# Performance work log

Measured on AMD Instinct MI355X. Metric: run time of the kernel, lower is better.

## Reference

```python
import jax, jax.numpy as jnp
import numpy as np

CHUNK = 128


def setup_inputs() -> dict:
    key = jax.random.key(0)
    ks = jax.random.split(key, 10)
    B, L, d, n = 4, 2048, 192, 64
    sd = 1.0 / np.sqrt(d)
    return {
        "x": jax.random.normal(ks[0], (B, L, d), dtype=jnp.float32),
        "A_log": -jnp.log(2.0) + 0.1 * jax.random.normal(ks[1], (d,), dtype=jnp.float32),
        "W_B": sd * jax.random.normal(ks[2], (n, d), dtype=jnp.float32),
        "W_C": sd * jax.random.normal(ks[3], (n, d), dtype=jnp.float32),
        "W_dt": sd * jax.random.normal(ks[4], (d, d), dtype=jnp.float32),
        "b_dt": 0.1 * jax.random.normal(ks[5], (d,), dtype=jnp.float32),
        "W_xp": sd * jax.random.normal(ks[6], (2 * d, d), dtype=jnp.float32),
        "b_xp": 0.1 * jax.random.normal(ks[7], (2 * d,), dtype=jnp.float32),
        "W_out": sd * jax.random.normal(ks[8], (d, d), dtype=jnp.float32),
        "b_out": 0.1 * jax.random.normal(ks[9], (d,), dtype=jnp.float32),
    }


def reference(x, A_log, W_B, W_C, W_dt, b_dt, W_xp, b_xp, W_out, b_out):
    p = CHUNK
    b, l, d = x.shape
    n = W_B.shape[0]
    pad = (-l) % p
    xp = jnp.pad(x, ((0, 0), (0, pad), (0, 0))) if pad > 0 else x
    c = xp.shape[1] // p

    A = -jnp.exp(A_log)                                   # (d,)
    proj = xp @ W_xp.T + b_xp                             # (b, Lp, 2d)
    x_bar, z = jnp.split(proj, 2, axis=-1)
    Bm = x_bar @ W_B.T                                    # (b, Lp, n)
    Cm = x_bar @ W_C.T                                    # (b, Lp, n)
    dt = jax.nn.softplus(x_bar @ W_dt.T + b_dt)           # (b, Lp, d)
    A_bar = jnp.exp(dt * A)                               # (b, Lp, d)

    resh = lambda t: t.reshape(b, c, p, t.shape[-1])
    xc, Bc, Cc, Ac = resh(x_bar), resh(Bm), resh(Cm), resh(A_bar)

    # intra-chunk: masked decay matrix M[b,c,i,j,d]
    log_A = jnp.log(jnp.abs(Ac) + 1e-8)
    la_cum = jnp.cumsum(log_A, axis=2)                    # (b,c,p,d)
    log_M = la_cum[:, :, :, None, :] - la_cum[:, :, None, :, :]
    causal = jnp.tril(jnp.ones((p, p), dtype=x.dtype))
    M = jnp.exp(log_M) * causal[None, None, :, :, None]   # (b,c,p,p,d)
    G = jnp.einsum('bcin,bcjn->bcij', Cc, Bc)             # C_i . B_j
    # same math as einsum('bcpn,bcpnd->bcpd', C, einsum('bcijd,bcjnd->bcind', M, B x))
    y_intra = jnp.einsum('bcij,bcijd,bcjd->bcid', G, M, xc)

    # inter-chunk recurrence over chunk states
    chunk_A = jnp.prod(Ac, axis=2)                        # (b,c,d)
    chunk_states = jnp.einsum('bcpn,bcpd->bcnd', Bc, xc * Ac)

    def step(state, inp):
        ca, cs = inp                                       # (b,d), (b,n,d)
        return state * ca[:, None, :] + cs, state          # emit state BEFORE update

    _, prev = jax.lax.scan(
        step,
        jnp.zeros((b, n, d), dtype=x.dtype),
        (jnp.moveaxis(chunk_A, 1, 0), jnp.moveaxis(chunk_states, 1, 0)),
    )
    prev = jnp.moveaxis(prev, 0, 1)                       # (b,c,n,d)
    y_inter = jnp.einsum('bcpn,bcnd->bcpd', Cc, prev)

    y = (y_intra + y_inter).reshape(b, c * p, d)[:, :l]
    y = y * jax.nn.silu(z[:, :l])
    return y @ W_out.T + b_out
```

## Files before the change

kernel.cpp:

```cpp
#include <hip/hip_runtime.h>
#include <math.h>

#define TOK      8192
#define DIM      192
#define NST      64
#define PCHUNK   128
#define NCHUNKS  64
#define CPB      16
#define BATCH    4
#define NG       4
#define NPG      16
#define SUB      32
#define NSUB     4

typedef __attribute__((ext_vector_type(8))) short  bf16x8;
typedef __attribute__((ext_vector_type(4))) float  f32x4;

__device__ __forceinline__ unsigned short f2bf(float f) {
    unsigned int u = __float_as_uint(f);
    u += 0x7fff + ((u >> 16) & 1);
    return (unsigned short)(u >> 16);
}
__device__ __forceinline__ float bf2f(unsigned short h) {
    return __uint_as_float(((unsigned int)h) << 16);
}

__global__ __launch_bounds__(256)
void cast_kernel(const float* __restrict__ x,   const float* __restrict__ Wxp,
                 const float* __restrict__ WB,  const float* __restrict__ WC,
                 const float* __restrict__ Wdt, const float* __restrict__ Wout,
                 unsigned short* __restrict__ xb,     unsigned short* __restrict__ wxpb,
                 unsigned short* __restrict__ wbcdtb, unsigned short* __restrict__ woutb)
{
    int u = blockIdx.x * 256 + threadIdx.x;
    const float* src; unsigned short* dst; int idx;
    if      (u < 393216) { src = x;    dst = xb;             idx = u; }
    else if (u < 411648) { src = Wxp;  dst = wxpb;           idx = u - 393216; }
    else if (u < 414720) { src = WB;   dst = wbcdtb;         idx = u - 411648; }
    else if (u < 417792) { src = WC;   dst = wbcdtb + 12288; idx = u - 414720; }
    else if (u < 427008) { src = Wdt;  dst = wbcdtb + 24576; idx = u - 417792; }
    else if (u < 436224) { src = Wout; dst = woutb;          idx = u - 427008; }
    else return;
    float4 v = *(const float4*)(src + (size_t)idx * 4);
    ushort4 r; r.x = f2bf(v.x); r.y = f2bf(v.y); r.z = f2bf(v.z); r.w = f2bf(v.w);
    *(ushort4*)(dst + (size_t)idx * 4) = r;
}

__device__ __forceinline__
void mfma_64x64(const unsigned short* __restrict__ X, int ldx,
                const unsigned short* __restrict__ W, int K,
                int m_wave, int n0, int lr, int kg, f32x4 acc[4][4])
{
    for (int k0 = 0; k0 < K; k0 += 32) {
        bf16x8 af[4], bfr[4];
        #pragma unroll
        for (int mi = 0; mi < 4; ++mi)
            af[mi] = *(const bf16x8*)(X + (size_t)(m_wave + mi*16 + lr) * ldx + k0 + kg*8);
        #pragma unroll
        for (int ni = 0; ni < 4; ++ni)
            bfr[ni] = *(const bf16x8*)(W + (size_t)(n0 + ni*16 + lr) * K + k0 + kg*8);
        #pragma unroll
        for (int mi = 0; mi < 4; ++mi)
            #pragma unroll
            for (int ni = 0; ni < 4; ++ni)
                acc[mi][ni] = __builtin_amdgcn_mfma_f32_16x16x32_bf16(
                                  af[mi], bfr[ni], acc[mi][ni], 0, 0, 0);
    }
}

__global__ __launch_bounds__(256)
void proj_gemm(const unsigned short* __restrict__ xb,
               const unsigned short* __restrict__ wxpb,
               const float* __restrict__ b_xp,
               float* __restrict__ proj, unsigned short* __restrict__ projb)
{
    const int lane = threadIdx.x & 63, wave = threadIdx.x >> 6;
    const int m_wave = blockIdx.x * 256 + wave * 64;
    const int n0 = blockIdx.y * 64;
    const int lr = lane & 15, kg = lane >> 4;
    f32x4 acc[4][4] = {};
    mfma_64x64(xb, DIM, wxpb, DIM, m_wave, n0, lr, kg, acc);
    #pragma unroll
    for (int ni = 0; ni < 4; ++ni) {
        int col = n0 + ni*16 + lr;
        float bias = b_xp[col];
        #pragma unroll
        for (int mi = 0; mi < 4; ++mi)
            #pragma unroll
            for (int r = 0; r < 4; ++r) {
                int row = m_wave + mi*16 + kg*4 + r;
                float v = acc[mi][ni][r] + bias;
                proj [(size_t)row * 384 + col] = v;
                projb[(size_t)row * 384 + col] = f2bf(v);
            }
    }
}

__global__ __launch_bounds__(256)
void bcdt_gemm(const unsigned short* __restrict__ projb,
               const unsigned short* __restrict__ wbcdtb,
               const float* __restrict__ b_dt, const float* __restrict__ A_log,
               float* __restrict__ BC, float* __restrict__ Abar)
{
    const int lane = threadIdx.x & 63, wave = threadIdx.x >> 6;
    const int m_wave = blockIdx.x * 256 + wave * 64;
    const int n0 = blockIdx.y * 64;
    const int lr = lane & 15, kg = lane >> 4;
    f32x4 acc[4][4] = {};
    mfma_64x64(projb, 384, wbcdtb, DIM, m_wave, n0, lr, kg, acc);
    if (n0 < 128) {
        #pragma unroll
        for (int ni = 0; ni < 4; ++ni) {
            int col = n0 + ni*16 + lr;
            #pragma unroll
            for (int mi = 0; mi < 4; ++mi)
                #pragma unroll
                for (int r = 0; r < 4; ++r) {
                    int row = m_wave + mi*16 + kg*4 + r;
                    BC[(size_t)row * 128 + col] = acc[mi][ni][r];
                }
        }
    } else {
        #pragma unroll
        for (int ni = 0; ni < 4; ++ni) {
            int c2 = n0 - 128 + ni*16 + lr;
            float bias = b_dt[c2];
            float Av = -expf(A_log[c2]);
            #pragma unroll
            for (int mi = 0; mi < 4; ++mi)
                #pragma unroll
                for (int r = 0; r < 4; ++r) {
                    int row = m_wave + mi*16 + kg*4 + r;
                    float v = acc[mi][ni][r] + bias;
                    float sp = (v > 20.f) ? v : log1pf(expf(v));
                    Abar[(size_t)row * DIM + c2] = expf(sp * Av);
                }
        }
    }
}

__global__ __launch_bounds__(256)
void out_gemm(const unsigned short* __restrict__ ygb,
              const unsigned short* __restrict__ woutb,
              const float* __restrict__ b_out, float* __restrict__ out)
{
    const int lane = threadIdx.x & 63, wave = threadIdx.x >> 6;
    const int m_wave = blockIdx.x * 256 + wave * 64;
    const int n0 = blockIdx.y * 64;
    const int lr = lane & 15, kg = lane >> 4;
    f32x4 acc[4][4] = {};
    mfma_64x64(ygb, DIM, woutb, DIM, m_wave, n0, lr, kg, acc);
    #pragma unroll
    for (int ni = 0; ni < 4; ++ni) {
        int col = n0 + ni*16 + lr;
        float bias = b_out[col];
        #pragma unroll
        for (int mi = 0; mi < 4; ++mi)
            #pragma unroll
            for (int r = 0; r < 4; ++r) {
                int row = m_wave + mi*16 + kg*4 + r;
                out[(size_t)row * DIM + col] = acc[mi][ni][r] + bias;
            }
    }
}

__global__ __launch_bounds__(256)
void chunkstate_kernel(const float* __restrict__ proj,
                       const float* __restrict__ Abar,
                       const float* __restrict__ Bm,
                       float* __restrict__ cs_part)
{
    int bc = blockIdx.x, ps = blockIdx.y;
    int t0 = bc * PCHUNK + ps * 32;
    __shared__ float Bs[32][68];
    __shared__ float xAs[32][200];
    for (int idx = threadIdx.x; idx < 32 * NST; idx += 256) {
        int p = idx >> 6, nn = idx & 63;
        Bs[p][nn] = Bm[(size_t)(t0 + p) * 128 + nn];
    }
    for (int idx = threadIdx.x; idx < 32 * DIM; idx += 256) {
        int p = idx / DIM, dd = idx % DIM;
        int t = t0 + p;
        xAs[p][dd] = proj[(size_t)t * 384 + dd] * Abar[(size_t)t * DIM + dd];
    }
    __syncthreads();
    const int tx = threadIdx.x & 15;
    const int ty = threadIdx.x >> 4;
    float acc[4][12] = {};
    for (int p = 0; p < 32; ++p) {
        float bb[4], xa[12];
        #pragma unroll
        for (int q = 0; q < 4; ++q)  bb[q] = Bs[p][ty * 4 + q];
        #pragma unroll
        for (int r = 0; r < 12; ++r) xa[r] = xAs[p][tx * 12 + r];
        #pragma unroll
        for (int q = 0; q < 4; ++q)
            #pragma unroll
            for (int r = 0; r < 12; ++r)
                acc[q][r] = fmaf(bb[q], xa[r], acc[q][r]);
    }
    size_t base = ((size_t)ps * NCHUNKS + bc) * NST * DIM;
    #pragma unroll
    for (int q = 0; q < 4; ++q)
        #pragma unroll
        for (int r = 0; r < 12; ++r)
            cs_part[base + (size_t)(ty * 4 + q) * DIM + tx * 12 + r] = acc[q][r];
}

__global__ __launch_bounds__(192)
void sub_state_kernel(const float* __restrict__ proj,
                      const float* __restrict__ Abar,
                      const float* __restrict__ Bm,
                      float* __restrict__ S,
                      float* __restrict__ dprod)
{
    int bc = blockIdx.x, s = blockIdx.y, g = blockIdx.z;
    int dd = threadIdx.x;
    int t0 = bc * PCHUNK + s * SUB;
    __shared__ float Bs[SUB][NPG];
    for (int idx = threadIdx.x; idx < SUB * NPG; idx += 192) {
        int i = idx / NPG, j = idx % NPG;
        Bs[i][j] = Bm[(size_t)(t0 + i) * 128 + g * NPG + j];
    }
    __syncthreads();
    float H[NPG] = {};
    float cp = 1.f;
    float a_cur = fabsf(Abar[(size_t)t0 * DIM + dd]) + 1e-8f;
    float x_cur = proj[(size_t)t0 * 384 + dd];
    for (int i = 0; i < SUB; ++i) {
        float a_nxt = 0.f, x_nxt = 0.f;
        if (i + 1 < SUB) {
            a_nxt = fabsf(Abar[(size_t)(t0 + i + 1) * DIM + dd]) + 1e-8f;
            x_nxt = proj[(size_t)(t0 + i + 1) * 384 + dd];
        }
        cp *= a_cur;
        #pragma unroll
        for (int j = 0; j < NPG; ++j)
            H[j] = fmaf(H[j], a_cur, Bs[i][j] * x_cur);
        a_cur = a_nxt; x_cur = x_nxt;
    }
    size_t base = ((size_t)(bc * NSUB + s) * NST + g * NPG) * DIM + dd;
    #pragma unroll
    for (int j = 0; j < NPG; ++j)
        S[base + (size_t)j * DIM] = H[j];
    if (g == 0) dprod[(size_t)(bc * NSUB + s) * DIM + dd] = cp;
}

__global__ __launch_bounds__(256)
void scan_kernel(const float* __restrict__ dprod,
                 const float* __restrict__ cs_part,
                 float* __restrict__ prev)
{
    int idx = blockIdx.x * 256 + threadIdx.x;
    if (idx >= BATCH * NST * DIM) return;
    int dd = idx % DIM;
    int nn = (idx / DIM) % NST;
    int b  = idx / (DIM * NST);
    const size_t Q = (size_t)NCHUNKS * NST * DIM;
    float st = 0.f;
    for (int c = 0; c < CPB; ++c) {
        int bc = b * CPB + c;
        size_t off = ((size_t)bc * NST + nn) * DIM + dd;
        prev[off] = st;
        float cA = dprod[(size_t)(bc*NSUB+0) * DIM + dd]
                 * dprod[(size_t)(bc*NSUB+1) * DIM + dd]
                 * dprod[(size_t)(bc*NSUB+2) * DIM + dd]
                 * dprod[(size_t)(bc*NSUB+3) * DIM + dd];
        float sum = cs_part[off] + cs_part[off + Q] + cs_part[off + 2*Q] + cs_part[off + 3*Q];
        st = fmaf(st, cA, sum);
    }
}

__global__ __launch_bounds__(256)
void sub_scan_kernel(const float* __restrict__ S,
                     const float* __restrict__ dprod,
                     float* __restrict__ carry)
{
    int v = blockIdx.x * 256 + threadIdx.x;
    if (v >= NCHUNKS * NST * 48) return;
    int dd = (v % 48) * 4;
    int nn = (v / 48) % NST;
    int bc = v / (48 * NST);
    float4 st = {0.f, 0.f, 0.f, 0.f};
    #pragma unroll
    for (int s = 0; s < NSUB; ++s) {
        size_t off = ((size_t)(bc * NSUB + s) * NST + nn) * DIM + dd;
        *(float4*)(carry + off) = st;
        float4 dp = *(const float4*)(dprod + (size_t)(bc * NSUB + s) * DIM + dd);
        float4 Sv = *(const float4*)(S + off);
        st.x = fmaf(st.x, dp.x, Sv.x);
        st.y = fmaf(st.y, dp.y, Sv.y);
        st.z = fmaf(st.z, dp.z, Sv.z);
        st.w = fmaf(st.w, dp.w, Sv.w);
    }
}

__global__ __launch_bounds__(192)
void intra_kernel(const float* __restrict__ proj,
                  const float* __restrict__ Abar,
                  const float* __restrict__ Bm,
                  const float* __restrict__ Cm,
                  const float* __restrict__ prev,
                  const float* __restrict__ carry,
                  float* __restrict__ p_y)
{
    int bc = blockIdx.x, s = blockIdx.y, g = blockIdx.z;
    int dd = threadIdx.x;
    int t0 = bc * PCHUNK + s * SUB;
    __shared__ float Bs[SUB][NPG];
    __shared__ float Cs[SUB][NPG];
    for (int idx = threadIdx.x; idx < SUB * NPG; idx += 192) {
        int i = idx / NPG, j = idx % NPG;
        Bs[i][j] = Bm[(size_t)(t0 + i) * 128 + g * NPG + j];
        Cs[i][j] = Cm[(size_t)(t0 + i) * 128 + g * NPG + j];
    }
    float H[NPG], P[NPG], CI[NPG];
    #pragma unroll
    for (int j = 0; j < NPG; ++j) {
        H[j] = 0.f;
        P[j]  = prev[((size_t)bc * NST + g * NPG + j) * DIM + dd];
        CI[j] = carry[((size_t)(bc * NSUB + s) * NST + g * NPG + j) * DIM + dd];
    }
    __syncthreads();

    float cp = 1.f;
    float a_cur = fabsf(Abar[(size_t)t0 * DIM + dd]) + 1e-8f;
    float x_cur = proj[(size_t)t0 * 384 + dd];
    for (int i = 0; i < SUB; ++i) {
        int t = t0 + i;
        float a_nxt = 0.f, x_nxt = 0.f;
        if (i + 1 < SUB) {
            a_nxt = fabsf(Abar[(size_t)(t + 1) * DIM + dd]) + 1e-8f;
            x_nxt = proj[(size_t)(t + 1) * 384 + dd];
        }
        cp *= a_cur;
        float ya[4] = {0.f, 0.f, 0.f, 0.f};
        #pragma unroll
        for (int j = 0; j < NPG; ++j) {
            H[j] = fmaf(H[j], a_cur, Bs[i][j] * x_cur);
            float full = fmaf(cp, CI[j], H[j]) + P[j];
            ya[j & 3] = fmaf(Cs[i][j], full, ya[j & 3]);
        }
        p_y[((size_t)g * TOK + t) * DIM + dd] = (ya[0] + ya[1]) + (ya[2] + ya[3]);
        a_cur = a_nxt; x_cur = x_nxt;
    }
}

__global__ __launch_bounds__(256)
void gate_kernel(const float* __restrict__ p_y,
                 const float* __restrict__ proj,
                 unsigned short* __restrict__ ygb)
{
    int v = blockIdx.x * 256 + threadIdx.x;
    if (v >= TOK * 48) return;
    int t = v / 48;
    int dd = (v % 48) * 4;
    const size_t Q = (size_t)TOK * DIM;
    size_t off = (size_t)t * DIM + dd;
    float4 y0 = *(const float4*)(p_y + off);
    float4 y1 = *(const float4*)(p_y + off + Q);
    float4 y2 = *(const float4*)(p_y + off + 2*Q);
    float4 y3 = *(const float4*)(p_y + off + 3*Q);
    float4 z  = *(const float4*)(proj + (size_t)t * 384 + DIM + dd);
    ushort4 r;
    r.x = f2bf((y0.x+y1.x+y2.x+y3.x) * (z.x / (1.f + expf(-z.x))));
    r.y = f2bf((y0.y+y1.y+y2.y+y3.y) * (z.y / (1.f + expf(-z.y))));
    r.z = f2bf((y0.z+y1.z+y2.z+y3.z) * (z.z / (1.f + expf(-z.z))));
    r.w = f2bf((y0.w+y1.w+y2.w+y3.w) * (z.w / (1.f + expf(-z.w))));
    *(ushort4*)(ygb + off) = r;
}

extern "C" void kernel_launch(void* const* d_in, const int* in_sizes, int n_in,
                              void* d_out, int out_size, void* d_ws, size_t ws_size,
                              hipStream_t stream)
{
    (void)in_sizes; (void)n_in; (void)out_size; (void)ws_size;
    const float* x     = (const float*)d_in[0];
    const float* A_log = (const float*)d_in[1];
    const float* W_B   = (const float*)d_in[2];
    const float* W_C   = (const float*)d_in[3];
    const float* W_dt  = (const float*)d_in[4];
    const float* b_dt  = (const float*)d_in[5];
    const float* W_xp  = (const float*)d_in[6];
    const float* b_xp  = (const float*)d_in[7];
    const float* W_out = (const float*)d_in[8];
    const float* b_out = (const float*)d_in[9];
    float* out = (float*)d_out;

    char* w = (char*)d_ws;
    auto take = [&](size_t bytes) { char* p = w; w += (bytes + 255) & ~(size_t)255; return p; };
    float*          proj   = (float*)         take((size_t)TOK*384*4);
    unsigned short* projb  = (unsigned short*)take((size_t)TOK*384*2);
    unsigned short* xb     = (unsigned short*)take((size_t)TOK*DIM*2);
    unsigned short* wxpb   = (unsigned short*)take((size_t)384*DIM*2);
    unsigned short* wbcdtb = (unsigned short*)take((size_t)320*DIM*2);
    unsigned short* woutb  = (unsigned short*)take((size_t)DIM*DIM*2);
    float*          BC     = (float*)         take((size_t)TOK*128*4);
    float*          Abar   = (float*)         take((size_t)TOK*DIM*4);
    float*          dprod  = (float*)         take((size_t)NCHUNKS*NSUB*DIM*4);
    float*          prev   = (float*)         take((size_t)NCHUNKS*NST*DIM*4);
    float*          csc    = (float*)         take((size_t)4*NCHUNKS*NST*DIM*4);
    float*          p_y    = (float*)         take((size_t)NG*TOK*DIM*4);
    unsigned short* ygb    = (unsigned short*)take((size_t)TOK*DIM*2);
    float* S     = p_y;
    float* carry = csc;
    const float* Bm = BC;
    const float* Cm = BC + 64;

    dim3 blk(256);

    cast_kernel<<<dim3((436224 + 255)/256), blk, 0, stream>>>(
        x, W_xp, W_B, W_C, W_dt, W_out, xb, wxpb, wbcdtb, woutb);
    proj_gemm<<<dim3(TOK/256, 384/64), blk, 0, stream>>>(xb, wxpb, b_xp, proj, projb);
    bcdt_gemm<<<dim3(TOK/256, 320/64), blk, 0, stream>>>(projb, wbcdtb, b_dt, A_log, BC, Abar);
    chunkstate_kernel<<<dim3(NCHUNKS, NSUB), blk, 0, stream>>>(proj, Abar, Bm, csc);
    sub_state_kernel<<<dim3(NCHUNKS, NSUB, NG), dim3(192), 0, stream>>>(
        proj, Abar, Bm, S, dprod);
    scan_kernel<<<dim3((BATCH*NST*DIM + 255)/256), blk, 0, stream>>>(dprod, csc, prev);
    sub_scan_kernel<<<dim3((NCHUNKS*NST*48 + 255)/256), blk, 0, stream>>>(S, dprod, carry);
    intra_kernel<<<dim3(NCHUNKS, NSUB, NG), dim3(192), 0, stream>>>(
        proj, Abar, Bm, Cm, prev, carry, p_y);
    gate_kernel<<<dim3((TOK*48 + 255)/256), blk, 0, stream>>>(p_y, proj, ygb);
    out_gemm<<<dim3(TOK/256, DIM/64), blk, 0, stream>>>(ygb, woutb, b_out, out);
}
```

Baseline: 200.9 us.

## Fuse chunk-state GEMM into sub-chunk state scan and drop sub-scan kernel

Removes the separate chunkstate GEMM kernel by having the sub-chunk recurrence kernel also accumulate the decay-weighted chunk-state contributions (R) alongside the sub-chunk states. The sub-scan kernel is folded into the intra kernel, which rebuilds its carry-in state from the stored sub-chunk states and decay products. The scan kernel is vectorised with float4 and sums the per-sub-chunk R parts. The state grouping goes from 4 groups of 16 to 2 groups of 32, which halves the partial-output traffic to the gate kernel but doubles per-thread register state and the serial work per block.

```diff
diff --git a/kernel.cpp b/kernel.cpp
--- a/kernel.cpp
+++ b/kernel.cpp
@@ -8,10 +8,10 @@
 #define NCHUNKS  64
 #define CPB      16
 #define BATCH    4
-#define NG       4
-#define NPG      16
 #define SUB      32
 #define NSUB     4
+#define NG2      2
+#define NPG2     32
 
 typedef __attribute__((ext_vector_type(8))) short  bf16x8;
 typedef __attribute__((ext_vector_type(4))) float  f32x4;
@@ -20,9 +20,6 @@
     unsigned int u = __float_as_uint(f);
     u += 0x7fff + ((u >> 16) & 1);
     return (unsigned short)(u >> 16);
-}
-__device__ __forceinline__ float bf2f(unsigned short h) {
-    return __uint_as_float(((unsigned int)h) << 16);
 }
 
 __global__ __launch_bounds__(256)
@@ -164,66 +161,24 @@
     }
 }
 
-__global__ __launch_bounds__(256)
-void chunkstate_kernel(const float* __restrict__ proj,
-                       const float* __restrict__ Abar,
-                       const float* __restrict__ Bm,
-                       float* __restrict__ cs_part)
-{
-    int bc = blockIdx.x, ps = blockIdx.y;
-    int t0 = bc * PCHUNK + ps * 32;
-    __shared__ float Bs[32][68];
-    __shared__ float xAs[32][200];
-    for (int idx = threadIdx.x; idx < 32 * NST; idx += 256) {
-        int p = idx >> 6, nn = idx & 63;
-        Bs[p][nn] = Bm[(size_t)(t0 + p) * 128 + nn];
-    }
-    for (int idx = threadIdx.x; idx < 32 * DIM; idx += 256) {
-        int p = idx / DIM, dd = idx % DIM;
-        int t = t0 + p;
-        xAs[p][dd] = proj[(size_t)t * 384 + dd] * Abar[(size_t)t * DIM + dd];
-    }
-    __syncthreads();
-    const int tx = threadIdx.x & 15;
-    const int ty = threadIdx.x >> 4;
-    float acc[4][12] = {};
-    for (int p = 0; p < 32; ++p) {
-        float bb[4], xa[12];
-        #pragma unroll
-        for (int q = 0; q < 4; ++q)  bb[q] = Bs[p][ty * 4 + q];
-        #pragma unroll
-        for (int r = 0; r < 12; ++r) xa[r] = xAs[p][tx * 12 + r];
-        #pragma unroll
-        for (int q = 0; q < 4; ++q)
-            #pragma unroll
-            for (int r = 0; r < 12; ++r)
-                acc[q][r] = fmaf(bb[q], xa[r], acc[q][r]);
-    }
-    size_t base = ((size_t)ps * NCHUNKS + bc) * NST * DIM;
-    #pragma unroll
-    for (int q = 0; q < 4; ++q)
-        #pragma unroll
-        for (int r = 0; r < 12; ++r)
-            cs_part[base + (size_t)(ty * 4 + q) * DIM + tx * 12 + r] = acc[q][r];
-}
-
 __global__ __launch_bounds__(192)
-void sub_state_kernel(const float* __restrict__ proj,
-                      const float* __restrict__ Abar,
-                      const float* __restrict__ Bm,
-                      float* __restrict__ S,
-                      float* __restrict__ dprod)
+void state_kernel(const float* __restrict__ proj,
+                  const float* __restrict__ Abar,
+                  const float* __restrict__ Bm,
+                  float* __restrict__ S,
+                  float* __restrict__ R,
+                  float* __restrict__ dprod)
 {
     int bc = blockIdx.x, s = blockIdx.y, g = blockIdx.z;
     int dd = threadIdx.x;
     int t0 = bc * PCHUNK + s * SUB;
-    __shared__ float Bs[SUB][NPG];
-    for (int idx = threadIdx.x; idx < SUB * NPG; idx += 192) {
-        int i = idx / NPG, j = idx % NPG;
-        Bs[i][j] = Bm[(size_t)(t0 + i) * 128 + g * NPG + j];
+    __shared__ float Bs[SUB][NPG2];
+    for (int idx = threadIdx.x; idx < SUB * NPG2; idx += 192) {
+        int i = idx >> 5, j = idx & 31;
+        Bs[i][j] = Bm[(size_t)(t0 + i) * 128 + g * NPG2 + j];
     }
     __syncthreads();
-    float H[NPG] = {};
+    float H[NPG2] = {}, Rr[NPG2] = {};
     float cp = 1.f;
     float a_cur = fabsf(Abar[(size_t)t0 * DIM + dd]) + 1e-8f;
     float x_cur = proj[(size_t)t0 * 384 + dd];
@@ -235,63 +190,52 @@
         }
         cp *= a_cur;
         #pragma unroll
-        for (int j = 0; j < NPG; ++j)
-            H[j] = fmaf(H[j], a_cur, Bs[i][j] * x_cur);
+        for (int j = 0; j < NPG2; ++j) {
+            float u = Bs[i][j] * x_cur;
+            H[j]  = fmaf(a_cur, H[j], u);
+            Rr[j] = fmaf(u, a_cur, Rr[j]);
+        }
         a_cur = a_nxt; x_cur = x_nxt;
     }
-    size_t base = ((size_t)(bc * NSUB + s) * NST + g * NPG) * DIM + dd;
+    size_t base = (((size_t)(bc * NSUB + s)) * NST + g * NPG2) * DIM + dd;
     #pragma unroll
-    for (int j = 0; j < NPG; ++j)
+    for (int j = 0; j < NPG2; ++j) {
         S[base + (size_t)j * DIM] = H[j];
+        R[base + (size_t)j * DIM] = Rr[j];
+    }
     if (g == 0) dprod[(size_t)(bc * NSUB + s) * DIM + dd] = cp;
 }
 
 __global__ __launch_bounds__(256)
 void scan_kernel(const float* __restrict__ dprod,
-                 const float* __restrict__ cs_part,
+                 const float* __restrict__ R,
                  float* __restrict__ prev)
 {
-    int idx = blockIdx.x * 256 + threadIdx.x;
-    if (idx >= BATCH * NST * DIM) return;
-    int dd = idx % DIM;
-    int nn = (idx / DIM) % NST;
-    int b  = idx / (DIM * NST);
-    const size_t Q = (size_t)NCHUNKS * NST * DIM;
-    float st = 0.f;
+    int v = blockIdx.x * 256 + threadIdx.x;
+    if (v >= BATCH * NST * 48) return;
+    int dd = (v % 48) * 4;
+    int nn = (v / 48) % NST;
+    int b  = v / (48 * NST);
+    const size_t Q2 = (size_t)NST * DIM;
+    float4 st = {0.f, 0.f, 0.f, 0.f};
     for (int c = 0; c < CPB; ++c) {
         int bc = b * CPB + c;
-        size_t off = ((size_t)bc * NST + nn) * DIM + dd;
-        prev[off] = st;
-        float cA = dprod[(size_t)(bc*NSUB+0) * DIM + dd]
-                 * dprod[(size_t)(bc*NSUB+1) * DIM + dd]
-                 * dprod[(size_t)(bc*NSUB+2) * DIM + dd]
-                 * dprod[(size_t)(bc*NSUB+3) * DIM + dd];
-        float sum = cs_part[off] + cs_part[off + Q] + cs_part[off + 2*Q] + cs_part[off + 3*Q];
-        st = fmaf(st, cA, sum);
-    }
-}
-
-__global__ __launch_bounds__(256)
-void sub_scan_kernel(const float* __restrict__ S,
-                     const float* __restrict__ dprod,
-                     float* __restrict__ carry)
-{
-    int v = blockIdx.x * 256 + threadIdx.x;
-    if (v >= NCHUNKS * NST * 48) return;
-    int dd = (v % 48) * 4;
-    int nn = (v / 48) % NST;
-    int bc = v / (48 * NST);
-    float4 st = {0.f, 0.f, 0.f, 0.f};
-    #pragma unroll
-    for (int s = 0; s < NSUB; ++s) {
-        size_t off = ((size_t)(bc * NSUB + s) * NST + nn) * DIM + dd;
-        *(float4*)(carry + off) = st;
-        float4 dp = *(const float4*)(dprod + (size_t)(bc * NSUB + s) * DIM + dd);
-        float4 Sv = *(const float4*)(S + off);
-        st.x = fmaf(st.x, dp.x, Sv.x);
-        st.y = fmaf(st.y, dp.y, Sv.y);
-        st.z = fmaf(st.z, dp.z, Sv.z);
-        st.w = fmaf(st.w, dp.w, Sv.w);
+        size_t so = ((size_t)(bc * NSUB) * NST + nn) * DIM + dd;
+        float4 Rs = {0.f, 0.f, 0.f, 0.f};
+        float4 cA = {1.f, 1.f, 1.f, 1.f};
+        #pragma unroll
+        for (int s = 0; s < NSUB; ++s) {
+            float4 dp = *(const float4*)(dprod + (size_t)(bc * NSUB + s) * DIM + dd);
+            float4 Rv = *(const float4*)(R + so + (size_t)s * Q2);
+            cA.x *= dp.x; cA.y *= dp.y; cA.z *= dp.z; cA.w *= dp.w;
+            Rs.x += Rv.x; Rs.y += Rv.y; Rs.z += Rv.z; Rs.w += Rv.w;
+        }
+        size_t po = ((size_t)bc * NST + nn) * DIM + dd;
+        *(float4*)(prev + po) = st;
+        st.x = fmaf(st.x, cA.x, Rs.x);
+        st.y = fmaf(st.y, cA.y, Rs.y);
+        st.z = fmaf(st.z, cA.z, Rs.z);
+        st.w = fmaf(st.w, cA.w, Rs.w);
     }
 }
 
@@ -301,29 +245,33 @@
                   const float* __restrict__ Bm,
                   const float* __restrict__ Cm,
                   const float* __restrict__ prev,
-                  const float* __restrict__ carry,
+                  const float* __restrict__ S,
+                  const float* __restrict__ dprod,
                   float* __restrict__ p_y)
 {
     int bc = blockIdx.x, s = blockIdx.y, g = blockIdx.z;
     int dd = threadIdx.x;
     int t0 = bc * PCHUNK + s * SUB;
-    __shared__ float Bs[SUB][NPG];
-    __shared__ float Cs[SUB][NPG];
-    for (int idx = threadIdx.x; idx < SUB * NPG; idx += 192) {
-        int i = idx / NPG, j = idx % NPG;
-        Bs[i][j] = Bm[(size_t)(t0 + i) * 128 + g * NPG + j];
-        Cs[i][j] = Cm[(size_t)(t0 + i) * 128 + g * NPG + j];
-    }
-    float H[NPG], P[NPG], CI[NPG];
+    __shared__ float Bs[SUB][NPG2];
+    __shared__ float Cs[SUB][NPG2];
+    for (int idx = threadIdx.x; idx < SUB * NPG2; idx += 192) {
+        int i = idx >> 5, j = idx & 31;
+        Bs[i][j] = Bm[(size_t)(t0 + i) * 128 + g * NPG2 + j];
+        Cs[i][j] = Cm[(size_t)(t0 + i) * 128 + g * NPG2 + j];
+    }
+    float H[NPG2] = {}, P[NPG2];
+    for (int k = 0; k < s; ++k) {
+        float dpk = dprod[(size_t)(bc * NSUB + k) * DIM + dd];
+        size_t sb = (((size_t)(bc * NSUB + k)) * NST + g * NPG2) * DIM + dd;
+        #pragma unroll
+        for (int j = 0; j < NPG2; ++j)
+            H[j] = fmaf(H[j], dpk, S[sb + (size_t)j * DIM]);
+    }
     #pragma unroll
-    for (int j = 0; j < NPG; ++j) {
-        H[j] = 0.f;
-        P[j]  = prev[((size_t)bc * NST + g * NPG + j) * DIM + dd];
-        CI[j] = carry[((size_t)(bc * NSUB + s) * NST + g * NPG + j) * DIM + dd];
-    }
+    for (int j = 0; j < NPG2; ++j)
+        P[j] = prev[((size_t)bc * NST + g * NPG2 + j) * DIM + dd];
     __syncthreads();
 
-    float cp = 1.f;
     float a_cur = fabsf(Abar[(size_t)t0 * DIM + dd]) + 1e-8f;
     float x_cur = proj[(size_t)t0 * 384 + dd];
     for (int i = 0; i < SUB; ++i) {
@@ -333,13 +281,12 @@
             a_nxt = fabsf(Abar[(size_t)(t + 1) * DIM + dd]) + 1e-8f;
             x_nxt = proj[(size_t)(t + 1) * 384 + dd];
         }
-        cp *= a_cur;
         float ya[4] = {0.f, 0.f, 0.f, 0.f};
         #pragma unroll
-        for (int j = 0; j < NPG; ++j) {
-            H[j] = fmaf(H[j], a_cur, Bs[i][j] * x_cur);
-            float full = fmaf(cp, CI[j], H[j]) + P[j];
-            ya[j & 3] = fmaf(Cs[i][j], full, ya[j & 3]);
+        for (int j = 0; j < NPG2; ++j) {
+            float u = Bs[i][j] * x_cur;
+            H[j] = fmaf(a_cur, H[j], u);
+            ya[j & 3] = fmaf(Cs[i][j], H[j] + P[j], ya[j & 3]);
         }
         p_y[((size_t)g * TOK + t) * DIM + dd] = (ya[0] + ya[1]) + (ya[2] + ya[3]);
         a_cur = a_nxt; x_cur = x_nxt;
@@ -359,14 +306,12 @@
     size_t off = (size_t)t * DIM + dd;
     float4 y0 = *(const float4*)(p_y + off);
     float4 y1 = *(const float4*)(p_y + off + Q);
-    float4 y2 = *(const float4*)(p_y + off + 2*Q);
-    float4 y3 = *(const float4*)(p_y + off + 3*Q);
     float4 z  = *(const float4*)(proj + (size_t)t * 384 + DIM + dd);
     ushort4 r;
-    r.x = f2bf((y0.x+y1.x+y2.x+y3.x) * (z.x / (1.f + expf(-z.x))));
-    r.y = f2bf((y0.y+y1.y+y2.y+y3.y) * (z.y / (1.f + expf(-z.y))));
-    r.z = f2bf((y0.z+y1.z+y2.z+y3.z) * (z.z / (1.f + expf(-z.z))));
-    r.w = f2bf((y0.w+y1.w+y2.w+y3.w) * (z.w / (1.f + expf(-z.w))));
+    r.x = f2bf((y0.x+y1.x) * (z.x / (1.f + expf(-z.x))));
+    r.y = f2bf((y0.y+y1.y) * (z.y / (1.f + expf(-z.y))));
+    r.z = f2bf((y0.z+y1.z) * (z.z / (1.f + expf(-z.z))));
+    r.w = f2bf((y0.w+y1.w) * (z.w / (1.f + expf(-z.w))));
     *(ushort4*)(ygb + off) = r;
 }
 
@@ -399,11 +344,10 @@
     float*          Abar   = (float*)         take((size_t)TOK*DIM*4);
     float*          dprod  = (float*)         take((size_t)NCHUNKS*NSUB*DIM*4);
     float*          prev   = (float*)         take((size_t)NCHUNKS*NST*DIM*4);
-    float*          csc    = (float*)         take((size_t)4*NCHUNKS*NST*DIM*4);
-    float*          p_y    = (float*)         take((size_t)NG*TOK*DIM*4);
+    float*          Sarr   = (float*)         take((size_t)NCHUNKS*NSUB*NST*DIM*4);
+    float*          Rarr   = (float*)         take((size_t)NCHUNKS*NSUB*NST*DIM*4);
+    float*          p_y    = (float*)         take((size_t)NG2*TOK*DIM*4);
     unsigned short* ygb    = (unsigned short*)take((size_t)TOK*DIM*2);
-    float* S     = p_y;
-    float* carry = csc;
     const float* Bm = BC;
     const float* Cm = BC + 64;
 
@@ -413,13 +357,11 @@
         x, W_xp, W_B, W_C, W_dt, W_out, xb, wxpb, wbcdtb, woutb);
     proj_gemm<<<dim3(TOK/256, 384/64), blk, 0, stream>>>(xb, wxpb, b_xp, proj, projb);
     bcdt_gemm<<<dim3(TOK/256, 320/64), blk, 0, stream>>>(projb, wbcdtb, b_dt, A_log, BC, Abar);
-    chunkstate_kernel<<<dim3(NCHUNKS, NSUB), blk, 0, stream>>>(proj, Abar, Bm, csc);
-    sub_state_kernel<<<dim3(NCHUNKS, NSUB, NG), dim3(192), 0, stream>>>(
-        proj, Abar, Bm, S, dprod);
-    scan_kernel<<<dim3((BATCH*NST*DIM + 255)/256), blk, 0, stream>>>(dprod, csc, prev);
-    sub_scan_kernel<<<dim3((NCHUNKS*NST*48 + 255)/256), blk, 0, stream>>>(S, dprod, carry);
-    intra_kernel<<<dim3(NCHUNKS, NSUB, NG), dim3(192), 0, stream>>>(
-        proj, Abar, Bm, Cm, prev, carry, p_y);
+    state_kernel<<<dim3(NCHUNKS, NSUB, NG2), dim3(192), 0, stream>>>(
+        proj, Abar, Bm, Sarr, Rarr, dprod);
+    scan_kernel<<<dim3((BATCH*NST*48 + 255)/256), blk, 0, stream>>>(dprod, Rarr, prev);
+    intra_kernel<<<dim3(NCHUNKS, NSUB, NG2), dim3(192), 0, stream>>>(
+        proj, Abar, Bm, Cm, prev, Sarr, dprod, p_y);
     gate_kernel<<<dim3((TOK*48 + 255)/256), blk, 0, stream>>>(p_y, proj, ygb);
     out_gemm<<<dim3(TOK/256, DIM/64), blk, 0, stream>>>(ygb, woutb, b_out, out);
 }
```

Result: faster. 188.3 us (-6.3%).
